# Performance work log

Measured on AMD Instinct MI355X. Metric: run time of the kernel, lower is better.

The kernel has to match this reference:

```python
import jax, jax.numpy as jnp
import numpy as np

EPS = 1e-5

def bn2d(x, gamma, beta, mean, var):
    # eval-mode BatchNorm2d over channel dim 1
    scale = gamma * jax.lax.rsqrt(var + EPS)
    return (x - mean[None, :, None, None]) * scale[None, :, None, None] + beta[None, :, None, None]

def setup_inputs() -> dict:
    key = jax.random.key(0)
    ks = jax.random.split(key, 24)
    B, C, T, V = 128, 128, 64, 25
    R, O = C // 8, 256
    f = jax.random.normal
    inp = {
        "g1": f(ks[0], (B, C, T, V), jnp.float32),
        "h2": f(ks[1], (B, C, T // 2, V), jnp.float32),
        "As_r": jax.random.uniform(ks[2], (B, V, V), jnp.float32),
        "At_r": jax.random.uniform(ks[3], (B, T, T), jnp.float32),
        "sc1_w": f(ks[4], (R, C), jnp.float32) * 0.05,
        "sc1_b": jnp.zeros((R,), jnp.float32),
        "sc2_w": f(ks[5], (R, C), jnp.float32) * 0.05,
        "sc2_b": jnp.zeros((R,), jnp.float32),
        "tc1_w": f(ks[6], (R, C), jnp.float32) * 0.05,
        "tc1_b": jnp.zeros((R,), jnp.float32),
        "tc2_w": f(ks[7], (R, C), jnp.float32) * 0.05,
        "tc2_b": jnp.zeros((R,), jnp.float32),
        "act_s": jnp.ones((V, V), jnp.float32),
        "act_t": jnp.ones((T, T), jnp.float32),
        "sp_w": f(ks[8], (C, C), jnp.float32) * 0.05,
        "sp_b": jnp.zeros((C,), jnp.float32),
        "sp_gamma": jnp.ones((C,), jnp.float32),
        "sp_beta": jnp.zeros((C,), jnp.float32),
        "sp_mean": jnp.zeros((C,), jnp.float32),
        "sp_var": jnp.ones((C,), jnp.float32),
        "W1_w": f(ks[9], (O, 2 * C), jnp.float32) * 0.05,
        "W1_b": jnp.zeros((O,), jnp.float32),
        "W2_w": f(ks[10], (O, 2 * C), jnp.float32) * 0.05,
        "W2_b": jnp.zeros((O,), jnp.float32),
        "bn_gamma": jnp.ones((O,), jnp.float32),
        "bn_beta": jnp.zeros((O,), jnp.float32),
        "bn_mean": jnp.zeros((O,), jnp.float32),
        "bn_var": jnp.ones((O,), jnp.float32),
    }
    return inp

def reference(g1, h2, As_r, At_r, sc1_w, sc1_b, sc2_w, sc2_b, tc1_w, tc1_b, tc2_w, tc2_b,
              act_s, act_t, sp_w, sp_b, sp_gamma, sp_beta, sp_mean, sp_var,
              W1_w, W1_b, W2_w, W2_b, bn_gamma, bn_beta, bn_mean, bn_var):
    # get_As: mean over time -> 1x1 convs (pure channel matmuls) -> b x V x V attention
    sf = jnp.mean(g1, axis=2)                                   # [b,c,v]
    s1 = jnp.einsum('rc,bcv->bvr', sc1_w, sf) + sc1_b           # [b,v,r]
    s2 = jnp.einsum('rc,bcv->brv', sc2_w, sf) + sc2_b[None, :, None]
    As_at = jax.nn.relu(jnp.tanh(jnp.einsum('bvr,bru->bvu', s1, s2)))
    # get_At: mean over joints -> b x T x T attention
    tf = jnp.mean(g1, axis=3)                                   # [b,c,t]
    t1 = jnp.einsum('rc,bct->btr', tc1_w, tf) + tc1_b           # [b,t,r]
    t2 = jnp.einsum('rc,bct->brt', tc2_w, tf) + tc2_b[None, :, None]
    At_at = jax.nn.relu(jnp.tanh(jnp.einsum('btr,bry->bty', t1, t2)))

    As_act = As_r * act_s
    At_act = At_r * act_t
    As = As_at + As_act
    At = At_at + At_act

    nu1 = jnp.einsum('buv,bctv->bctu', As, g1)                  # spatial mixing
    nu1 = jnp.einsum('bctu,bty->bcyu', nu1, At)                 # temporal mixing

    # stride_pro: 1x1 conv, temporal stride 2, then BN (unit_tcn)
    nu1 = nu1[:, :, ::2, :]
    nu1 = jnp.einsum('oc,bctv->botv', sp_w, nu1) + sp_b[None, :, None, None]
    nu1 = bn2d(nu1, sp_gamma, sp_beta, sp_mean, sp_var)

    h_star2 = jnp.concatenate([nu1, h2], axis=1)                # [b,2c,t/2,v]
    a = jnp.einsum('oc,bctv->botv', W1_w, h_star2) + W1_b[None, :, None, None]
    g = jnp.einsum('oc,bctv->botv', W2_w, h_star2) + W2_b[None, :, None, None]
    g2 = bn2d(a * jax.nn.sigmoid(g), bn_gamma, bn_beta, bn_mean, bn_var)
    return (g2, As_at, At_at, As_act, At_act)
```

## Files before the change

### kernel.cpp

```cpp
#include <hip/hip_runtime.h>
#include <cstdint>
#include <cstddef>

typedef __attribute__((ext_vector_type(8))) short short8;
typedef __attribute__((ext_vector_type(4))) float f32x4;

#define EPSF 1e-5f

__device__ __forceinline__ unsigned short f2bf(float f) {
  union { float f; unsigned u; } v; v.f = f;
  unsigned r = v.u + 0x7FFFu + ((v.u >> 16) & 1u);
  return (unsigned short)(r >> 16);
}

__global__ __launch_bounds__(256) void k_means_tr(
    const float* __restrict__ g1, float* __restrict__ sf, float* __restrict__ tf,
    unsigned short* __restrict__ g1vt) {
  __shared__ __align__(16) float tile[1600];
  int bc = blockIdx.x;
  const float4* src = (const float4*)(g1 + (size_t)bc * 1600);
  float4* dst = (float4*)tile;
  for (int i = threadIdx.x; i < 400; i += 256) dst[i] = src[i];
  __syncthreads();
  int t = threadIdx.x;
  if (t < 64) {
    float s = 0.f;
    #pragma unroll
    for (int v = 0; v < 25; ++v) s += tile[t * 25 + v];
    tf[(size_t)bc * 64 + t] = s * (1.f / 25.f);
  } else if (t < 89) {
    int v = t - 64;
    float s = 0.f;
    for (int tt = 0; tt < 64; ++tt) s += tile[tt * 25 + v];
    sf[(size_t)bc * 25 + v] = s * (1.f / 64.f);
  }
  for (int p = threadIdx.x; p < 800; p += 256) {
    int j = p * 2;
    int v = j >> 6, tt = j & 63;
    unsigned short lo = f2bf(tile[tt * 25 + v]);
    unsigned short hi = f2bf(tile[(tt + 1) * 25 + v]);
    unsigned pack = (unsigned)lo | ((unsigned)hi << 16);
    *((unsigned*)(g1vt + (size_t)bc * 1600 + j)) = pack;
  }
}

__global__ __launch_bounds__(256) void k_spat(
    const float* __restrict__ sf, const float* __restrict__ sc1_w, const float* __restrict__ sc1_b,
    const float* __restrict__ sc2_w, const float* __restrict__ sc2_b,
    const float* __restrict__ As_r, const float* __restrict__ act_s,
    float* __restrict__ As_ws, float* __restrict__ out_As_at, float* __restrict__ out_As_act) {
  __shared__ float sfl[3200], w1[2048], w2[2048], s1[400], s2[400];
  int b = blockIdx.x;
  for (int i = threadIdx.x; i < 3200; i += 256) sfl[i] = sf[(size_t)b * 3200 + i];
  for (int i = threadIdx.x; i < 2048; i += 256) { w1[i] = sc1_w[i]; w2[i] = sc2_w[i]; }
  __syncthreads();
  for (int i = threadIdx.x; i < 800; i += 256) {
    if (i < 400) {
      int v = i >> 4, r = i & 15;
      float s = sc1_b[r];
      for (int c = 0; c < 128; ++c) s += w1[r * 128 + c] * sfl[c * 25 + v];
      s1[v * 16 + r] = s;
    } else {
      int j = i - 400;
      int r = j / 25, u = j % 25;
      float s = sc2_b[r];
      for (int c = 0; c < 128; ++c) s += w2[r * 128 + c] * sfl[c * 25 + u];
      s2[r * 25 + u] = s;
    }
  }
  __syncthreads();
  for (int i = threadIdx.x; i < 625; i += 256) {
    int v = i / 25, u = i % 25;
    float d = 0.f;
    #pragma unroll
    for (int r = 0; r < 16; ++r) d += s1[v * 16 + r] * s2[r * 25 + u];
    float at = d > 0.f ? tanhf(d) : 0.f;
    float act = As_r[(size_t)b * 625 + i] * act_s[i];
    out_As_at[(size_t)b * 625 + i] = at;
    out_As_act[(size_t)b * 625 + i] = act;
    As_ws[(size_t)b * 625 + i] = at + act;
  }
}

__global__ __launch_bounds__(256) void k_temp(
    const float* __restrict__ tf, const float* __restrict__ tc1_w, const float* __restrict__ tc1_b,
    const float* __restrict__ tc2_w, const float* __restrict__ tc2_b,
    const float* __restrict__ At_r, const float* __restrict__ act_t,
    float* __restrict__ Atev_ws, float* __restrict__ out_At_at, float* __restrict__ out_At_act) {
  __shared__ float tfl[8192], w1[2048], w2[2048], t1[1024], t2[1024];
  int b = blockIdx.x;
  for (int i = threadIdx.x; i < 8192; i += 256) tfl[i] = tf[(size_t)b * 8192 + i];
  for (int i = threadIdx.x; i < 2048; i += 256) { w1[i] = tc1_w[i]; w2[i] = tc2_w[i]; }
  __syncthreads();
  for (int i = threadIdx.x; i < 2048; i += 256) {
    if (i < 1024) {
      int t = i >> 4, r = i & 15;
      float s = tc1_b[r];
      for (int c = 0; c < 128; ++c) s += w1[r * 128 + c] * tfl[c * 64 + t];
      t1[t * 16 + r] = s;
    } else {
      int j = i - 1024;
      int r = j >> 6, t = j & 63;
      float s = tc2_b[r];
      for (int c = 0; c < 128; ++c) s += w2[r * 128 + c] * tfl[c * 64 + t];
      t2[r * 64 + t] = s;
    }
  }
  __syncthreads();
  for (int i = threadIdx.x; i < 4096; i += 256) {
    int t = i >> 6, y = i & 63;
    float d = 0.f;
    #pragma unroll
    for (int r = 0; r < 16; ++r) d += t1[t * 16 + r] * t2[r * 64 + y];
    float at = d > 0.f ? tanhf(d) : 0.f;
    float act = At_r[(size_t)b * 4096 + i] * act_t[i];
    out_At_at[(size_t)b * 4096 + i] = at;
    out_At_act[(size_t)b * 4096 + i] = act;
    if ((y & 1) == 0)
      Atev_ws[(size_t)b * 2048 + (y >> 1) * 64 + t] = at + act;
  }
}

__global__ __launch_bounds__(256) void k_prep(
    const float* __restrict__ W1_w, const float* __restrict__ W1_b,
    const float* __restrict__ W2_w, const float* __restrict__ W2_b,
    const float* __restrict__ sp_w, const float* __restrict__ sp_b,
    const float* __restrict__ sp_gamma, const float* __restrict__ sp_beta,
    const float* __restrict__ sp_mean, const float* __restrict__ sp_var,
    const float* __restrict__ bn_gamma, const float* __restrict__ bn_beta,
    const float* __restrict__ bn_mean, const float* __restrict__ bn_var,
    unsigned short* __restrict__ Wc1, unsigned short* __restrict__ Wc2,
    float* __restrict__ b1p, float* __restrict__ b2p,
    float* __restrict__ bnsc, float* __restrict__ bnsh) {
  __shared__ float w1row[256], w2row[256], scale[128], shift[128];
  int o = blockIdx.x;
  int t = threadIdx.x;
  w1row[t] = W1_w[o * 256 + t];
  w2row[t] = W2_w[o * 256 + t];
  if (t < 128) {
    float sc = sp_gamma[t] * rsqrtf(sp_var[t] + EPSF);
    scale[t] = sc;
    shift[t] = (sp_b[t] - sp_mean[t]) * sc + sp_beta[t];
  }
  __syncthreads();
  if (t < 128) {
    float a1 = 0.f, a2 = 0.f;
    for (int c = 0; c < 128; ++c) {
      float sw = sp_w[c * 128 + t];
      a1 += w1row[c] * scale[c] * sw;
      a2 += w2row[c] * scale[c] * sw;
    }
    Wc1[o * 256 + t] = f2bf(a1);
    Wc2[o * 256 + t] = f2bf(a2);
  } else {
    Wc1[o * 256 + t] = f2bf(w1row[t]);
    Wc2[o * 256 + t] = f2bf(w2row[t]);
  }
  if (t == 0) {
    float s = 0.f;
    for (int c = 0; c < 128; ++c) s += w1row[c] * shift[c];
    b1p[o] = W1_b[o] + s;
    float bs = bn_gamma[o] * rsqrtf(bn_var[o] + EPSF);
    bnsc[o] = bs;
    bnsh[o] = bn_beta[o] - bn_mean[o] * bs;
  } else if (t == 1) {
    float s = 0.f;
    for (int c = 0; c < 128; ++c) s += w2row[c] * shift[c];
    b2p[o] = W2_b[o] + s;
  }
}

__global__ __launch_bounds__(256) void k_nu2(
    const unsigned short* __restrict__ g1vt, const float* __restrict__ Atev,
    const float* __restrict__ As_ws, unsigned short* __restrict__ nu2) {
  __shared__ __align__(16) unsigned short At_l[32 * 72];
  __shared__ __align__(16) unsigned short As_l[32 * 40];
  __shared__ __align__(16) unsigned short P2_l[8 * 32 * 40];
  int blk = blockIdx.x;
  int b = blk >> 4;
  int c0 = (blk & 15) * 8;
  int tid = threadIdx.x;
  int w = tid >> 6, l = tid & 63;
  for (int i = tid; i < 2048; i += 256)
    At_l[(i >> 6) * 72 + (i & 63)] = f2bf(Atev[(size_t)b * 2048 + i]);
  for (int i = tid; i < 1280; i += 256) As_l[i] = 0;
  for (int i = tid; i < 10240; i += 256) P2_l[i] = 0;
  __syncthreads();
  for (int i = tid; i < 625; i += 256)
    As_l[(i / 25) * 40 + (i % 25)] = f2bf(As_ws[(size_t)b * 625 + i]);
  __syncthreads();

  short8 afr[2][2];
  #pragma unroll
  for (int mi = 0; mi < 2; ++mi)
    #pragma unroll
    for (int ks = 0; ks < 2; ++ks) {
      int y = mi * 16 + (l & 15);
      int tt = ks * 32 + (l >> 4) * 8;
      afr[mi][ks] = *(const short8*)(At_l + y * 72 + tt);
    }
  for (int nt = w; nt < 13; nt += 4) {
    int n = nt * 16 + (l & 15);
    int nc = n < 200 ? n : 199;
    int cc = nc / 25, vv = nc % 25;
    const unsigned short* gp = g1vt + ((size_t)(b * 128 + c0 + cc) * 25 + vv) * 64;
    short8 bfr[2];
    #pragma unroll
    for (int ks = 0; ks < 2; ++ks)
      bfr[ks] = *(const short8*)(gp + ks * 32 + (l >> 4) * 8);
    #pragma unroll
    for (int mi = 0; mi < 2; ++mi) {
      f32x4 acc = {0.f, 0.f, 0.f, 0.f};
      acc = __builtin_amdgcn_mfma_f32_16x16x32_bf16(afr[mi][0], bfr[0], acc, 0, 0, 0);
      acc = __builtin_amdgcn_mfma_f32_16x16x32_bf16(afr[mi][1], bfr[1], acc, 0, 0, 0);
      if (n < 200) {
        #pragma unroll
        for (int r = 0; r < 4; ++r) {
          int y = mi * 16 + (l >> 4) * 4 + r;
          P2_l[cc * 1280 + y * 40 + vv] = f2bf(acc[r]);
        }
      }
    }
  }
  __syncthreads();

  for (int cw = w; cw < 8; cw += 4) {
    #pragma unroll
    for (int mi = 0; mi < 2; ++mi) {
      int y = mi * 16 + (l & 15);
      short8 a2 = *(const short8*)(P2_l + cw * 1280 + y * 40 + (l >> 4) * 8);
      #pragma unroll
      for (int nt2 = 0; nt2 < 2; ++nt2) {
        int u = nt2 * 16 + (l & 15);
        short8 b2 = *(const short8*)(As_l + u * 40 + (l >> 4) * 8);
        f32x4 acc = {0.f, 0.f, 0.f, 0.f};
        acc = __builtin_amdgcn_mfma_f32_16x16x32_bf16(a2, b2, acc, 0, 0, 0);
        #pragma unroll
        for (int r = 0; r < 4; ++r) {
          int yy = mi * 16 + (l >> 4) * 4 + r;
          int uu = nt2 * 16 + (l & 15);
          if (uu < 25)
            nu2[(size_t)(b * 128 + c0 + cw) * 800 + yy * 25 + uu] = f2bf(acc[r]);
        }
      }
    }
  }
}

__global__ __launch_bounds__(512) void k_final(
    const unsigned short* __restrict__ nu2, const float* __restrict__ h2,
    const unsigned short* __restrict__ Wc1, const unsigned short* __restrict__ Wc2,
    const float* __restrict__ b1p, const float* __restrict__ b2p,
    const float* __restrict__ bnsc, const float* __restrict__ bnsh,
    float* __restrict__ g2) {
  __shared__ __align__(16) unsigned short x_l[32 * 264];
  int blk = blockIdx.x;
  int b = blk / 5;
  int pbase = (blk % 5) * 160;
  int tid = threadIdx.x;
  int w = tid >> 6, l = tid & 63;
  int lrow = l & 15, lgr = l >> 4;
  int ow0 = w * 32;

  short8 aw1[2][8], aw2[2][8];
  {
    const unsigned short* wr1 = Wc1 + (ow0 + lrow) * 256 + lgr * 8;
    const unsigned short* wr2 = Wc2 + (ow0 + lrow) * 256 + lgr * 8;
    #pragma unroll
    for (int mi = 0; mi < 2; ++mi)
      #pragma unroll
      for (int ks = 0; ks < 8; ++ks) {
        aw1[mi][ks] = *(const short8*)(wr1 + mi * 16 * 256 + ks * 32);
        aw2[mi][ks] = *(const short8*)(wr2 + mi * 16 * 256 + ks * 32);
      }
  }
  float b1v[2][4], b2v[2][4], scv[2][4], shv[2][4];
  #pragma unroll
  for (int mi = 0; mi < 2; ++mi)
    #pragma unroll
    for (int r = 0; r < 4; ++r) {
      int o = ow0 + mi * 16 + lgr * 4 + r;
      b1v[mi][r] = b1p[o];
      b2v[mi][r] = b2p[o];
      scv[mi][r] = bnsc[o];
      shv[mi][r] = bnsh[o];
    }

  int kA = tid >> 2;
  int pA = (tid & 3) * 8;
  const unsigned short* srcA = nu2 + ((size_t)b * 128 + kA) * 800 + pbase + pA;
  const float* srcB = h2 + ((size_t)b * 128 + kA) * 800 + pbase + pA;

  short8 cA;
  float4 cB0, cB1;
  cA = *(const short8*)srcA;
  cB0 = *(const float4*)srcB;
  cB1 = *(const float4*)(srcB + 4);

  for (int pt = 0; pt < 5; ++pt) {
    #pragma unroll
    for (int j = 0; j < 8; ++j)
      x_l[(pA + j) * 264 + kA] = (unsigned short)cA[j];
    x_l[(pA + 0) * 264 + 128 + kA] = f2bf(cB0.x);
    x_l[(pA + 1) * 264 + 128 + kA] = f2bf(cB0.y);
    x_l[(pA + 2) * 264 + 128 + kA] = f2bf(cB0.z);
    x_l[(pA + 3) * 264 + 128 + kA] = f2bf(cB0.w);
    x_l[(pA + 4) * 264 + 128 + kA] = f2bf(cB1.x);
    x_l[(pA + 5) * 264 + 128 + kA] = f2bf(cB1.y);
    x_l[(pA + 6) * 264 + 128 + kA] = f2bf(cB1.z);
    x_l[(pA + 7) * 264 + 128 + kA] = f2bf(cB1.w);
    __syncthreads();

    if (pt < 4) {
      cA = *(const short8*)(srcA + (pt + 1) * 32);
      cB0 = *(const float4*)(srcB + (pt + 1) * 32);
      cB1 = *(const float4*)(srcB + (pt + 1) * 32 + 4);
    }

    f32x4 vz = {0.f, 0.f, 0.f, 0.f};
    f32x4 acc1[2][2], acc2[2][2];
    #pragma unroll
    for (int mi = 0; mi < 2; ++mi)
      #pragma unroll
      for (int nf = 0; nf < 2; ++nf) { acc1[mi][nf] = vz; acc2[mi][nf] = vz; }
    #pragma unroll
    for (int ks = 0; ks < 8; ++ks) {
      int koff = ks * 32 + lgr * 8;
      short8 bf0 = *(const short8*)(x_l + lrow * 264 + koff);
      short8 bf1 = *(const short8*)(x_l + (16 + lrow) * 264 + koff);
      acc1[0][0] = __builtin_amdgcn_mfma_f32_16x16x32_bf16(aw1[0][ks], bf0, acc1[0][0], 0, 0, 0);
      acc1[0][1] = __builtin_amdgcn_mfma_f32_16x16x32_bf16(aw1[0][ks], bf1, acc1[0][1], 0, 0, 0);
      acc1[1][0] = __builtin_amdgcn_mfma_f32_16x16x32_bf16(aw1[1][ks], bf0, acc1[1][0], 0, 0, 0);
      acc1[1][1] = __builtin_amdgcn_mfma_f32_16x16x32_bf16(aw1[1][ks], bf1, acc1[1][1], 0, 0, 0);
      acc2[0][0] = __builtin_amdgcn_mfma_f32_16x16x32_bf16(aw2[0][ks], bf0, acc2[0][0], 0, 0, 0);
      acc2[0][1] = __builtin_amdgcn_mfma_f32_16x16x32_bf16(aw2[0][ks], bf1, acc2[0][1], 0, 0, 0);
      acc2[1][0] = __builtin_amdgcn_mfma_f32_16x16x32_bf16(aw2[1][ks], bf0, acc2[1][0], 0, 0, 0);
      acc2[1][1] = __builtin_amdgcn_mfma_f32_16x16x32_bf16(aw2[1][ks], bf1, acc2[1][1], 0, 0, 0);
    }

    int p0 = pbase + pt * 32;
    #pragma unroll
    for (int mi = 0; mi < 2; ++mi)
      #pragma unroll
      for (int r = 0; r < 4; ++r) {
        int o = ow0 + mi * 16 + lgr * 4 + r;
        float* gp = g2 + ((size_t)b * 256 + o) * 800 + p0 + lrow;
        #pragma unroll
        for (int nf = 0; nf < 2; ++nf) {
          float a = acc1[mi][nf][r] + b1v[mi][r];
          float g = acc2[mi][nf][r] + b2v[mi][r];
          float sig = 1.f / (1.f + __expf(-g));
          gp[nf * 16] = (a * sig) * scv[mi][r] + shv[mi][r];
        }
      }
    __syncthreads();
  }
}

extern "C" void kernel_launch(void* const* d_in, const int* in_sizes, int n_in,
                              void* d_out, int out_size, void* d_ws, size_t ws_size,
                              hipStream_t stream) {
  (void)in_sizes; (void)n_in; (void)out_size; (void)ws_size;
  const float* g1    = (const float*)d_in[0];
  const float* h2    = (const float*)d_in[1];
  const float* As_r  = (const float*)d_in[2];
  const float* At_r  = (const float*)d_in[3];
  const float* sc1_w = (const float*)d_in[4];
  const float* sc1_b = (const float*)d_in[5];
  const float* sc2_w = (const float*)d_in[6];
  const float* sc2_b = (const float*)d_in[7];
  const float* tc1_w = (const float*)d_in[8];
  const float* tc1_b = (const float*)d_in[9];
  const float* tc2_w = (const float*)d_in[10];
  const float* tc2_b = (const float*)d_in[11];
  const float* act_s = (const float*)d_in[12];
  const float* act_t = (const float*)d_in[13];
  const float* sp_w  = (const float*)d_in[14];
  const float* sp_b  = (const float*)d_in[15];
  const float* sp_gamma = (const float*)d_in[16];
  const float* sp_beta  = (const float*)d_in[17];
  const float* sp_mean  = (const float*)d_in[18];
  const float* sp_var   = (const float*)d_in[19];
  const float* W1_w = (const float*)d_in[20];
  const float* W1_b = (const float*)d_in[21];
  const float* W2_w = (const float*)d_in[22];
  const float* W2_b = (const float*)d_in[23];
  const float* bn_gamma = (const float*)d_in[24];
  const float* bn_beta  = (const float*)d_in[25];
  const float* bn_mean  = (const float*)d_in[26];
  const float* bn_var   = (const float*)d_in[27];

  float* out = (float*)d_out;
  float* out_g2     = out;
  float* out_As_at  = out + 26214400;
  float* out_At_at  = out + 26294400;
  float* out_As_act = out + 26818688;
  float* out_At_act = out + 26898688;

  char* ws = (char*)d_ws;
  float* sf    = (float*)(ws + 0);
  float* tf    = (float*)(ws + 1638400);
  float* As_ws = (float*)(ws + 5832704);
  float* Atev  = (float*)(ws + 6152704);
  unsigned short* Wc1 = (unsigned short*)(ws + 7201280);
  unsigned short* Wc2 = (unsigned short*)(ws + 7332352);
  float* b1pv  = (float*)(ws + 7463424);
  float* b2pv  = (float*)(ws + 7464448);
  float* bnscv = (float*)(ws + 7465472);
  float* bnshv = (float*)(ws + 7466496);
  unsigned short* g1vt = (unsigned short*)(ws + 7467520);
  unsigned short* nu2  = (unsigned short*)(ws + 59896320);

  k_means_tr<<<dim3(16384), dim3(256), 0, stream>>>(g1, sf, tf, g1vt);
  k_spat<<<dim3(128), dim3(256), 0, stream>>>(sf, sc1_w, sc1_b, sc2_w, sc2_b,
                                              As_r, act_s, As_ws, out_As_at, out_As_act);
  k_temp<<<dim3(128), dim3(256), 0, stream>>>(tf, tc1_w, tc1_b, tc2_w, tc2_b,
                                              At_r, act_t, Atev, out_At_at, out_At_act);
  k_prep<<<dim3(256), dim3(256), 0, stream>>>(W1_w, W1_b, W2_w, W2_b, sp_w, sp_b,
                                              sp_gamma, sp_beta, sp_mean, sp_var,
                                              bn_gamma, bn_beta, bn_mean, bn_var,
                                              Wc1, Wc2, b1pv, b2pv, bnscv, bnshv);
  k_nu2<<<dim3(2048), dim3(256), 0, stream>>>(g1vt, Atev, As_ws, nu2);
  k_final<<<dim3(640), dim3(512), 0, stream>>>(nu2, h2, Wc1, Wc2, b1pv, b2pv,
                                               bnscv, bnshv, out_g2);
}
```

Before: 407.6 us.

## Merge small attention/prep kernels, pre-pack bf16 attention, double-buffer final LDS

Combines the spatial-attention, temporal-attention and weight-prep kernels into one launch that picks its role from the block index. That launch now writes the attention matrices as padded bf16, so k_nu2 copies them into LDS directly instead of converting from fp32. k_final gets a double-buffered, XOR-swizzled LDS tile, which removes one barrier per iteration and is meant to cut bank conflicts. The costs are more shared memory in the merged kernel and a larger LDS footprint in k_final.

```diff
diff --git a/kernel.cpp b/kernel.cpp
--- a/kernel.cpp
+++ b/kernel.cpp
@@ -44,84 +44,14 @@
   }
 }
 
-__global__ __launch_bounds__(256) void k_spat(
-    const float* __restrict__ sf, const float* __restrict__ sc1_w, const float* __restrict__ sc1_b,
+__global__ __launch_bounds__(256) void k_small(
+    const float* __restrict__ sf, const float* __restrict__ tf,
+    const float* __restrict__ sc1_w, const float* __restrict__ sc1_b,
     const float* __restrict__ sc2_w, const float* __restrict__ sc2_b,
+    const float* __restrict__ tc1_w, const float* __restrict__ tc1_b,
+    const float* __restrict__ tc2_w, const float* __restrict__ tc2_b,
     const float* __restrict__ As_r, const float* __restrict__ act_s,
-    float* __restrict__ As_ws, float* __restrict__ out_As_at, float* __restrict__ out_As_act) {
-  __shared__ float sfl[3200], w1[2048], w2[2048], s1[400], s2[400];
-  int b = blockIdx.x;
-  for (int i = threadIdx.x; i < 3200; i += 256) sfl[i] = sf[(size_t)b * 3200 + i];
-  for (int i = threadIdx.x; i < 2048; i += 256) { w1[i] = sc1_w[i]; w2[i] = sc2_w[i]; }
-  __syncthreads();
-  for (int i = threadIdx.x; i < 800; i += 256) {
-    if (i < 400) {
-      int v = i >> 4, r = i & 15;
-      float s = sc1_b[r];
-      for (int c = 0; c < 128; ++c) s += w1[r * 128 + c] * sfl[c * 25 + v];
-      s1[v * 16 + r] = s;
-    } else {
-      int j = i - 400;
-      int r = j / 25, u = j % 25;
-      float s = sc2_b[r];
-      for (int c = 0; c < 128; ++c) s += w2[r * 128 + c] * sfl[c * 25 + u];
-      s2[r * 25 + u] = s;
-    }
-  }
-  __syncthreads();
-  for (int i = threadIdx.x; i < 625; i += 256) {
-    int v = i / 25, u = i % 25;
-    float d = 0.f;
-    #pragma unroll
-    for (int r = 0; r < 16; ++r) d += s1[v * 16 + r] * s2[r * 25 + u];
-    float at = d > 0.f ? tanhf(d) : 0.f;
-    float act = As_r[(size_t)b * 625 + i] * act_s[i];
-    out_As_at[(size_t)b * 625 + i] = at;
-    out_As_act[(size_t)b * 625 + i] = act;
-    As_ws[(size_t)b * 625 + i] = at + act;
-  }
-}
-
-__global__ __launch_bounds__(256) void k_temp(
-    const float* __restrict__ tf, const float* __restrict__ tc1_w, const float* __restrict__ tc1_b,
-    const float* __restrict__ tc2_w, const float* __restrict__ tc2_b,
     const float* __restrict__ At_r, const float* __restrict__ act_t,
-    float* __restrict__ Atev_ws, float* __restrict__ out_At_at, float* __restrict__ out_At_act) {
-  __shared__ float tfl[8192], w1[2048], w2[2048], t1[1024], t2[1024];
-  int b = blockIdx.x;
-  for (int i = threadIdx.x; i < 8192; i += 256) tfl[i] = tf[(size_t)b * 8192 + i];
-  for (int i = threadIdx.x; i < 2048; i += 256) { w1[i] = tc1_w[i]; w2[i] = tc2_w[i]; }
-  __syncthreads();
-  for (int i = threadIdx.x; i < 2048; i += 256) {
-    if (i < 1024) {
-      int t = i >> 4, r = i & 15;
-      float s = tc1_b[r];
-      for (int c = 0; c < 128; ++c) s += w1[r * 128 + c] * tfl[c * 64 + t];
-      t1[t * 16 + r] = s;
-    } else {
-      int j = i - 1024;
-      int r = j >> 6, t = j & 63;
-      float s = tc2_b[r];
-      for (int c = 0; c < 128; ++c) s += w2[r * 128 + c] * tfl[c * 64 + t];
-      t2[r * 64 + t] = s;
-    }
-  }
-  __syncthreads();
-  for (int i = threadIdx.x; i < 4096; i += 256) {
-    int t = i >> 6, y = i & 63;
-    float d = 0.f;
-    #pragma unroll
-    for (int r = 0; r < 16; ++r) d += t1[t * 16 + r] * t2[r * 64 + y];
-    float at = d > 0.f ? tanhf(d) : 0.f;
-    float act = At_r[(size_t)b * 4096 + i] * act_t[i];
-    out_At_at[(size_t)b * 4096 + i] = at;
-    out_At_act[(size_t)b * 4096 + i] = act;
-    if ((y & 1) == 0)
-      Atev_ws[(size_t)b * 2048 + (y >> 1) * 64 + t] = at + act;
-  }
-}
-
-__global__ __launch_bounds__(256) void k_prep(
     const float* __restrict__ W1_w, const float* __restrict__ W1_b,
     const float* __restrict__ W2_w, const float* __restrict__ W2_b,
     const float* __restrict__ sp_w, const float* __restrict__ sp_b,
@@ -129,50 +59,142 @@
     const float* __restrict__ sp_mean, const float* __restrict__ sp_var,
     const float* __restrict__ bn_gamma, const float* __restrict__ bn_beta,
     const float* __restrict__ bn_mean, const float* __restrict__ bn_var,
+    unsigned short* __restrict__ As_bf, unsigned short* __restrict__ At_bf,
+    float* __restrict__ out_As_at, float* __restrict__ out_As_act,
+    float* __restrict__ out_At_at, float* __restrict__ out_At_act,
     unsigned short* __restrict__ Wc1, unsigned short* __restrict__ Wc2,
     float* __restrict__ b1p, float* __restrict__ b2p,
     float* __restrict__ bnsc, float* __restrict__ bnsh) {
-  __shared__ float w1row[256], w2row[256], scale[128], shift[128];
-  int o = blockIdx.x;
-  int t = threadIdx.x;
-  w1row[t] = W1_w[o * 256 + t];
-  w2row[t] = W2_w[o * 256 + t];
-  if (t < 128) {
-    float sc = sp_gamma[t] * rsqrtf(sp_var[t] + EPSF);
-    scale[t] = sc;
-    shift[t] = (sp_b[t] - sp_mean[t]) * sc + sp_beta[t];
-  }
-  __syncthreads();
-  if (t < 128) {
-    float a1 = 0.f, a2 = 0.f;
-    for (int c = 0; c < 128; ++c) {
-      float sw = sp_w[c * 128 + t];
-      a1 += w1row[c] * scale[c] * sw;
-      a2 += w2row[c] * scale[c] * sw;
-    }
-    Wc1[o * 256 + t] = f2bf(a1);
-    Wc2[o * 256 + t] = f2bf(a2);
+  __shared__ __align__(16) float sm[14336];
+  int blk = blockIdx.x;
+  int tid = threadIdx.x;
+
+  if (blk < 128) {
+    int b = blk;
+    float* sfl = sm;
+    float* w1  = sm + 3200;
+    float* w2  = sm + 5248;
+    float* s1  = sm + 7296;
+    float* s2  = sm + 7696;
+    for (int i = tid; i < 3200; i += 256) sfl[i] = sf[(size_t)b * 3200 + i];
+    for (int i = tid; i < 2048; i += 256) { w1[i] = sc1_w[i]; w2[i] = sc2_w[i]; }
+    __syncthreads();
+    for (int i = tid; i < 800; i += 256) {
+      if (i < 400) {
+        int v = i >> 4, r = i & 15;
+        float s = sc1_b[r];
+        for (int c = 0; c < 128; ++c) s += w1[r * 128 + c] * sfl[c * 25 + v];
+        s1[v * 16 + r] = s;
+      } else {
+        int j = i - 400;
+        int r = j / 25, u = j % 25;
+        float s = sc2_b[r];
+        for (int c = 0; c < 128; ++c) s += w2[r * 128 + c] * sfl[c * 25 + u];
+        s2[r * 25 + u] = s;
+      }
+    }
+    __syncthreads();
+    for (int i = tid; i < 1280; i += 256) {
+      int v = i / 40, u = i % 40;
+      if (v < 25 && u < 25) {
+        int ii = v * 25 + u;
+        float d = 0.f;
+        #pragma unroll
+        for (int r = 0; r < 16; ++r) d += s1[v * 16 + r] * s2[r * 25 + u];
+        float at = d > 0.f ? tanhf(d) : 0.f;
+        float act = As_r[(size_t)b * 625 + ii] * act_s[ii];
+        out_As_at[(size_t)b * 625 + ii] = at;
+        out_As_act[(size_t)b * 625 + ii] = act;
+        As_bf[(size_t)b * 1280 + i] = f2bf(at + act);
+      } else {
+        As_bf[(size_t)b * 1280 + i] = 0;
+      }
+    }
+  } else if (blk < 256) {
+    int b = blk - 128;
+    float* tfl = sm;
+    float* w1  = sm + 8192;
+    float* w2  = sm + 10240;
+    float* t1  = sm + 12288;
+    float* t2  = sm + 13312;
+    for (int i = tid; i < 8192; i += 256) tfl[i] = tf[(size_t)b * 8192 + i];
+    for (int i = tid; i < 2048; i += 256) { w1[i] = tc1_w[i]; w2[i] = tc2_w[i]; }
+    __syncthreads();
+    for (int i = tid; i < 2048; i += 256) {
+      if (i < 1024) {
+        int t = i >> 4, r = i & 15;
+        float s = tc1_b[r];
+        for (int c = 0; c < 128; ++c) s += w1[r * 128 + c] * tfl[c * 64 + t];
+        t1[t * 16 + r] = s;
+      } else {
+        int j = i - 1024;
+        int r = j >> 6, t = j & 63;
+        float s = tc2_b[r];
+        for (int c = 0; c < 128; ++c) s += w2[r * 128 + c] * tfl[c * 64 + t];
+        t2[r * 64 + t] = s;
+      }
+    }
+    __syncthreads();
+    for (int i = tid; i < 4096; i += 256) {
+      int t = i >> 6, y = i & 63;
+      float d = 0.f;
+      #pragma unroll
+      for (int r = 0; r < 16; ++r) d += t1[t * 16 + r] * t2[r * 64 + y];
+      float at = d > 0.f ? tanhf(d) : 0.f;
+      float act = At_r[(size_t)b * 4096 + i] * act_t[i];
+      out_At_at[(size_t)b * 4096 + i] = at;
+      out_At_act[(size_t)b * 4096 + i] = act;
+      if ((y & 1) == 0)
+        At_bf[(size_t)b * 2304 + (y >> 1) * 72 + t] = f2bf(at + act);
+    }
+    for (int i = tid; i < 256; i += 256)
+      At_bf[(size_t)b * 2304 + (i >> 3) * 72 + 64 + (i & 7)] = 0;
   } else {
-    Wc1[o * 256 + t] = f2bf(w1row[t]);
-    Wc2[o * 256 + t] = f2bf(w2row[t]);
-  }
-  if (t == 0) {
-    float s = 0.f;
-    for (int c = 0; c < 128; ++c) s += w1row[c] * shift[c];
-    b1p[o] = W1_b[o] + s;
-    float bs = bn_gamma[o] * rsqrtf(bn_var[o] + EPSF);
-    bnsc[o] = bs;
-    bnsh[o] = bn_beta[o] - bn_mean[o] * bs;
-  } else if (t == 1) {
-    float s = 0.f;
-    for (int c = 0; c < 128; ++c) s += w2row[c] * shift[c];
-    b2p[o] = W2_b[o] + s;
+    int o = blk - 256;
+    float* w1row = sm;
+    float* w2row = sm + 256;
+    float* scale = sm + 512;
+    float* shift = sm + 640;
+    int t = tid;
+    w1row[t] = W1_w[o * 256 + t];
+    w2row[t] = W2_w[o * 256 + t];
+    if (t < 128) {
+      float sc = sp_gamma[t] * rsqrtf(sp_var[t] + EPSF);
+      scale[t] = sc;
+      shift[t] = (sp_b[t] - sp_mean[t]) * sc + sp_beta[t];
+    }
+    __syncthreads();
+    if (t < 128) {
+      float a1 = 0.f, a2 = 0.f;
+      for (int c = 0; c < 128; ++c) {
+        float sw = sp_w[c * 128 + t];
+        a1 += w1row[c] * scale[c] * sw;
+        a2 += w2row[c] * scale[c] * sw;
+      }
+      Wc1[o * 256 + t] = f2bf(a1);
+      Wc2[o * 256 + t] = f2bf(a2);
+    } else {
+      Wc1[o * 256 + t] = f2bf(w1row[t]);
+      Wc2[o * 256 + t] = f2bf(w2row[t]);
+    }
+    if (t == 0) {
+      float s = 0.f;
+      for (int c = 0; c < 128; ++c) s += w1row[c] * shift[c];
+      b1p[o] = W1_b[o] + s;
+      float bs = bn_gamma[o] * rsqrtf(bn_var[o] + EPSF);
+      bnsc[o] = bs;
+      bnsh[o] = bn_beta[o] - bn_mean[o] * bs;
+    } else if (t == 1) {
+      float s = 0.f;
+      for (int c = 0; c < 128; ++c) s += w2row[c] * shift[c];
+      b2p[o] = W2_b[o] + s;
+    }
   }
 }
 
 __global__ __launch_bounds__(256) void k_nu2(
-    const unsigned short* __restrict__ g1vt, const float* __restrict__ Atev,
-    const float* __restrict__ As_ws, unsigned short* __restrict__ nu2) {
+    const unsigned short* __restrict__ g1vt, const unsigned short* __restrict__ At_bf,
+    const unsigned short* __restrict__ As_bf, unsigned short* __restrict__ nu2) {
   __shared__ __align__(16) unsigned short At_l[32 * 72];
   __shared__ __align__(16) unsigned short As_l[32 * 40];
   __shared__ __align__(16) unsigned short P2_l[8 * 32 * 40];
@@ -181,13 +203,16 @@
   int c0 = (blk & 15) * 8;
   int tid = threadIdx.x;
   int w = tid >> 6, l = tid & 63;
-  for (int i = tid; i < 2048; i += 256)
-    At_l[(i >> 6) * 72 + (i & 63)] = f2bf(Atev[(size_t)b * 2048 + i]);
-  for (int i = tid; i < 1280; i += 256) As_l[i] = 0;
-  for (int i = tid; i < 10240; i += 256) P2_l[i] = 0;
-  __syncthreads();
-  for (int i = tid; i < 625; i += 256)
-    As_l[(i / 25) * 40 + (i % 25)] = f2bf(As_ws[(size_t)b * 625 + i]);
+  {
+    const unsigned* Atg = (const unsigned*)(At_bf + (size_t)b * 2304);
+    const unsigned* Asg = (const unsigned*)(As_bf + (size_t)b * 1280);
+    unsigned* Atl = (unsigned*)At_l;
+    unsigned* Asl = (unsigned*)As_l;
+    unsigned* P2u = (unsigned*)P2_l;
+    for (int i = tid; i < 1152; i += 256) Atl[i] = Atg[i];
+    for (int i = tid; i < 640; i += 256) Asl[i] = Asg[i];
+    for (int i = tid; i < 5120; i += 256) P2u[i] = 0;
+  }
   __syncthreads();
 
   short8 afr[2][2];
@@ -253,7 +278,7 @@
     const float* __restrict__ b1p, const float* __restrict__ b2p,
     const float* __restrict__ bnsc, const float* __restrict__ bnsh,
     float* __restrict__ g2) {
-  __shared__ __align__(16) unsigned short x_l[32 * 264];
+  __shared__ __align__(16) unsigned short x_l[2][32 * 264];
   int blk = blockIdx.x;
   int b = blk / 5;
   int pbase = (blk % 5) * 160;
@@ -288,6 +313,7 @@
 
   int kA = tid >> 2;
   int pA = (tid & 3) * 8;
+  int kswA = kA ^ pA;
   const unsigned short* srcA = nu2 + ((size_t)b * 128 + kA) * 800 + pbase + pA;
   const float* srcB = h2 + ((size_t)b * 128 + kA) * 800 + pbase + pA;
 
@@ -296,19 +322,25 @@
   cA = *(const short8*)srcA;
   cB0 = *(const float4*)srcB;
   cB1 = *(const float4*)(srcB + 4);
+  {
+    unsigned short* xb = x_l[0];
+    #pragma unroll
+    for (int j = 0; j < 8; ++j)
+      xb[(pA + j) * 264 + kswA] = (unsigned short)cA[j];
+    xb[(pA + 0) * 264 + 128 + kswA] = f2bf(cB0.x);
+    xb[(pA + 1) * 264 + 128 + kswA] = f2bf(cB0.y);
+    xb[(pA + 2) * 264 + 128 + kswA] = f2bf(cB0.z);
+    xb[(pA + 3) * 264 + 128 + kswA] = f2bf(cB0.w);
+    xb[(pA + 4) * 264 + 128 + kswA] = f2bf(cB1.x);
+    xb[(pA + 5) * 264 + 128 + kswA] = f2bf(cB1.y);
+    xb[(pA + 6) * 264 + 128 + kswA] = f2bf(cB1.z);
+    xb[(pA + 7) * 264 + 128 + kswA] = f2bf(cB1.w);
+  }
+
+  int sw0 = lrow & 8;
+  int sw1 = 16 | sw0;
 
   for (int pt = 0; pt < 5; ++pt) {
-    #pragma unroll
-    for (int j = 0; j < 8; ++j)
-      x_l[(pA + j) * 264 + kA] = (unsigned short)cA[j];
-    x_l[(pA + 0) * 264 + 128 + kA] = f2bf(cB0.x);
-    x_l[(pA + 1) * 264 + 128 + kA] = f2bf(cB0.y);
-    x_l[(pA + 2) * 264 + 128 + kA] = f2bf(cB0.z);
-    x_l[(pA + 3) * 264 + 128 + kA] = f2bf(cB0.w);
-    x_l[(pA + 4) * 264 + 128 + kA] = f2bf(cB1.x);
-    x_l[(pA + 5) * 264 + 128 + kA] = f2bf(cB1.y);
-    x_l[(pA + 6) * 264 + 128 + kA] = f2bf(cB1.z);
-    x_l[(pA + 7) * 264 + 128 + kA] = f2bf(cB1.w);
     __syncthreads();
 
     if (pt < 4) {
@@ -317,6 +349,7 @@
       cB1 = *(const float4*)(srcB + (pt + 1) * 32 + 4);
     }
 
+    const unsigned short* xb = x_l[pt & 1];
     f32x4 vz = {0.f, 0.f, 0.f, 0.f};
     f32x4 acc1[2][2], acc2[2][2];
     #pragma unroll
@@ -326,8 +359,8 @@
     #pragma unroll
     for (int ks = 0; ks < 8; ++ks) {
       int koff = ks * 32 + lgr * 8;
-      short8 bf0 = *(const short8*)(x_l + lrow * 264 + koff);
-      short8 bf1 = *(const short8*)(x_l + (16 + lrow) * 264 + koff);
+      short8 bf0 = *(const short8*)(xb + lrow * 264 + (koff ^ sw0));
+      short8 bf1 = *(const short8*)(xb + (16 + lrow) * 264 + (koff ^ sw1));
       acc1[0][0] = __builtin_amdgcn_mfma_f32_16x16x32_bf16(aw1[0][ks], bf0, acc1[0][0], 0, 0, 0);
       acc1[0][1] = __builtin_amdgcn_mfma_f32_16x16x32_bf16(aw1[0][ks], bf1, acc1[0][1], 0, 0, 0);
       acc1[1][0] = __builtin_amdgcn_mfma_f32_16x16x32_bf16(aw1[1][ks], bf0, acc1[1][0], 0, 0, 0);
@@ -338,13 +371,27 @@
       acc2[1][1] = __builtin_amdgcn_mfma_f32_16x16x32_bf16(aw2[1][ks], bf1, acc2[1][1], 0, 0, 0);
     }
 
+    if (pt < 4) {
+      unsigned short* xn = x_l[(pt + 1) & 1];
+      #pragma unroll
+      for (int j = 0; j < 8; ++j)
+        xn[(pA + j) * 264 + kswA] = (unsigned short)cA[j];
+      xn[(pA + 0) * 264 + 128 + kswA] = f2bf(cB0.x);
+      xn[(pA + 1) * 264 + 128 + kswA] = f2bf(cB0.y);
+      xn[(pA + 2) * 264 + 128 + kswA] = f2bf(cB0.z);
+      xn[(pA + 3) * 264 + 128 + kswA] = f2bf(cB0.w);
+      xn[(pA + 4) * 264 + 128 + kswA] = f2bf(cB1.x);
+      xn[(pA + 5) * 264 + 128 + kswA] = f2bf(cB1.y);
+      xn[(pA + 6) * 264 + 128 + kswA] = f2bf(cB1.z);
+      xn[(pA + 7) * 264 + 128 + kswA] = f2bf(cB1.w);
+    }
+
     int p0 = pbase + pt * 32;
     #pragma unroll
     for (int mi = 0; mi < 2; ++mi)
       #pragma unroll
       for (int r = 0; r < 4; ++r) {
-        int o = ow0 + mi * 16 + lgr * 4 + r;
-        float* gp = g2 + ((size_t)b * 256 + o) * 800 + p0 + lrow;
+        float* gp = g2 + ((size_t)b * 256 + ow0 + mi * 16 + lgr * 4 + r) * 800 + p0 + lrow;
         #pragma unroll
         for (int nf = 0; nf < 2; ++nf) {
           float a = acc1[mi][nf][r] + b1v[mi][r];
@@ -353,7 +400,6 @@
           gp[nf * 16] = (a * sig) * scv[mi][r] + shv[mi][r];
         }
       }
-    __syncthreads();
   }
 }
 
@@ -400,8 +446,8 @@
   char* ws = (char*)d_ws;
   float* sf    = (float*)(ws + 0);
   float* tf    = (float*)(ws + 1638400);
-  float* As_ws = (float*)(ws + 5832704);
-  float* Atev  = (float*)(ws + 6152704);
+  unsigned short* As_bf = (unsigned short*)(ws + 5832704);
+  unsigned short* At_bf = (unsigned short*)(ws + 6160384);
   unsigned short* Wc1 = (unsigned short*)(ws + 7201280);
   unsigned short* Wc2 = (unsigned short*)(ws + 7332352);
   float* b1pv  = (float*)(ws + 7463424);
@@ -412,15 +458,16 @@
   unsigned short* nu2  = (unsigned short*)(ws + 59896320);
 
   k_means_tr<<<dim3(16384), dim3(256), 0, stream>>>(g1, sf, tf, g1vt);
-  k_spat<<<dim3(128), dim3(256), 0, stream>>>(sf, sc1_w, sc1_b, sc2_w, sc2_b,
-                                              As_r, act_s, As_ws, out_As_at, out_As_act);
-  k_temp<<<dim3(128), dim3(256), 0, stream>>>(tf, tc1_w, tc1_b, tc2_w, tc2_b,
-                                              At_r, act_t, Atev, out_At_at, out_At_act);
-  k_prep<<<dim3(256), dim3(256), 0, stream>>>(W1_w, W1_b, W2_w, W2_b, sp_w, sp_b,
-                                              sp_gamma, sp_beta, sp_mean, sp_var,
-                                              bn_gamma, bn_beta, bn_mean, bn_var,
-                                              Wc1, Wc2, b1pv, b2pv, bnscv, bnshv);
-  k_nu2<<<dim3(2048), dim3(256), 0, stream>>>(g1vt, Atev, As_ws, nu2);
+  k_small<<<dim3(512), dim3(256), 0, stream>>>(sf, tf, sc1_w, sc1_b, sc2_w, sc2_b,
+                                               tc1_w, tc1_b, tc2_w, tc2_b,
+                                               As_r, act_s, At_r, act_t,
+                                               W1_w, W1_b, W2_w, W2_b, sp_w, sp_b,
+                                               sp_gamma, sp_beta, sp_mean, sp_var,
+                                               bn_gamma, bn_beta, bn_mean, bn_var,
+                                               As_bf, At_bf, out_As_at, out_As_act,
+                                               out_At_at, out_At_act,
+                                               Wc1, Wc2, b1pv, b2pv, bnscv, bnshv);
+  k_nu2<<<dim3(2048), dim3(256), 0, stream>>>(g1vt, At_bf, As_bf, nu2);
   k_final<<<dim3(640), dim3(512), 0, stream>>>(nu2, h2, Wc1, Wc2, b1pv, b2pv,
                                                bnscv, bnshv, out_g2);
 }
```

Result: faster. 377.5 us (-7.4%).
